# Performance work log

Hardware: AMD Instinct MI355X
Metric: run time of the kernel (lower is better)

Reference implementation:

```python
import jax, jax.numpy as jnp
import numpy as np

SOLVER_STEPS = 10
POINT_DIM = 2
CONTEXT_DIM = 128
HIDDEN_DIM = 256


def setup_inputs() -> dict:
    key = jax.random.key(0)
    ks = jax.random.split(key, 8)
    B, N = 64, 4096
    in_dim = POINT_DIM + 1 + CONTEXT_DIM  # 131
    std = 0.1  # torch nn.init.normal_(std=0.1)
    x = jax.random.normal(ks[0], (B, N, POINT_DIM), jnp.float32)
    context = jax.random.normal(ks[1], (B, CONTEXT_DIM), jnp.float32)
    w1 = std * jax.random.normal(ks[2], (in_dim, HIDDEN_DIM), jnp.float32)
    w2 = std * jax.random.normal(ks[3], (HIDDEN_DIM, HIDDEN_DIM), jnp.float32)
    w3 = std * jax.random.normal(ks[4], (HIDDEN_DIM, HIDDEN_DIM), jnp.float32)
    w4 = std * 0.1 * jax.random.normal(ks[5], (HIDDEN_DIM, POINT_DIM), jnp.float32)  # last layer weight * 0.1
    b1 = jnp.zeros((HIDDEN_DIM,), jnp.float32)
    b2 = jnp.zeros((HIDDEN_DIM,), jnp.float32)
    b3 = jnp.zeros((HIDDEN_DIM,), jnp.float32)
    b4 = jnp.zeros((POINT_DIM,), jnp.float32)
    return {"x": x, "context": context, "w1": w1, "b1": b1, "w2": w2, "b2": b2,
            "w3": w3, "b3": b3, "w4": w4, "b4": b4}


def _mlp(pts, t, ctx, w1, b1, w2, b2, w3, b3, w4, b4):
    # pts: [B,N,2], ctx: [B,N,C] -> velocity [B,N,2]
    B, N, _ = pts.shape
    t_vec = jnp.full((B, N, 1), t, dtype=pts.dtype)
    h = jnp.concatenate([pts, t_vec, ctx], axis=-1)
    h = jax.nn.silu(h @ w1 + b1)  # Swish == silu
    h = jax.nn.silu(h @ w2 + b2)
    h = jax.nn.silu(h @ w3 + b3)
    return h @ w4 + b4


def reference(x, context, w1, b1, w2, b2, w3, b3, w4, b4):
    B, N, D = x.shape
    ctx = jnp.broadcast_to(context[:, None, :], (B, N, context.shape[-1]))
    dt = jnp.asarray(1.0 / SOLVER_STEPS, x.dtype)
    ts = jnp.linspace(0.0, 1.0, SOLVER_STEPS + 1, dtype=x.dtype)[:SOLVER_STEPS]
    e0 = jnp.broadcast_to(jnp.array([1.0, 0.0], x.dtype), x.shape)
    e1 = jnp.broadcast_to(jnp.array([0.0, 1.0], x.dtype), x.shape)

    def step(carry, t_i):
        pts, log_det = carry
        f = lambda p: _mlp(p, t_i, ctx, w1, b1, w2, b2, w3, b3, w4, b4)
        # exact divergence = trace of per-point 2x2 Jacobian via two JVPs
        v, j0 = jax.jvp(f, (pts,), (e0,))
        _, j1 = jax.jvp(f, (pts,), (e1,))
        div = (j0[..., 0] + j1[..., 1])[..., None]  # [B,N,1]
        return (pts + v * dt, log_det + div * dt), None

    init = (x, jnp.zeros((B, N, 1), x.dtype))
    (final_pts, log_det), _ = jax.lax.scan(step, init, ts)
    final_log_det = log_det[..., 0].sum(axis=1, keepdims=True)  # [B,1]
    return final_pts, final_log_det
```

## Files before the change

kernel.cpp:

```cpp
#include <hip/hip_runtime.h>

typedef short bf16x8 __attribute__((ext_vector_type(8)));
typedef float f32x4 __attribute__((ext_vector_type(4)));
typedef float f32x16 __attribute__((ext_vector_type(16)));

#define AS 264
#define T0OFF (32 * AS)
#define T1OFF (64 * AS)

__device__ __forceinline__ unsigned short f2bf(float f) {
    union { float f; unsigned int u; } v; v.f = f;
    unsigned int u = v.u + 0x7FFFu + ((v.u >> 16) & 1u);
    return (unsigned short)(u >> 16);
}
__device__ __forceinline__ unsigned cvtpk(float a, float b) {
    unsigned r;
    asm("v_cvt_pk_bf16_f32 %0, %1, %2" : "=v"(r) : "v"(a), "v"(b));
    return r;
}
__device__ __forceinline__ float bf2f(unsigned int h) {
    union { unsigned int u; float f; } v; v.u = h << 16; return v.f;
}
__device__ __forceinline__ float sigm(float x) {
    return __builtin_amdgcn_rcpf(1.0f + __expf(-x));
}

struct f4s { float v[4]; };
__device__ __forceinline__ f4s ld4(const float* p) {
    float4 t = *(const float4*)p;
    f4s r; r.v[0] = t.x; r.v[1] = t.y; r.v[2] = t.z; r.v[3] = t.w; return r;
}


__global__ void k_base(const float* __restrict__ ctx,
                       const float* __restrict__ w1,
                       const float* __restrict__ b1,
                       float* __restrict__ base) {
    const int b = blockIdx.x, n = threadIdx.x;
    float acc = b1[n];
    for (int c = 0; c < 128; ++c)
        acc += ctx[b * 128 + c] * w1[(3 + c) * 256 + n];
    base[b * 256 + n] = acc;
}

__global__ void k_frag(const float* __restrict__ w,
                       unsigned short* __restrict__ wf) {
    const int t = blockIdx.x * blockDim.x + threadIdx.x;
    const int j = t & 7, lane = (t >> 3) & 63, hb = (t >> 9) & 7, kk = t >> 12;
    const int c = kk * 16 + (lane >> 5) * 8 + j;
    const int h = hb * 32 + (lane & 31);
    wf[t] = f2bf(w[c * 256 + h]);
}

__device__ __forceinline__ void do_gemm32(const unsigned short* __restrict__ wf,
                                          const unsigned short* Asl,
                                          int abase, int wub,
                                          f32x16& aP, f32x16& aT0, f32x16& aT1) {
    const bf16x8* __restrict__ wp = (const bf16x8*)wf;
    bf16x8 buf[4];
#pragma unroll
    for (int i = 0; i < 4; ++i) buf[i] = wp[wub + i * 512];
#pragma unroll 1
    for (int kk = 0; kk < 12; kk += 4) {
#pragma unroll
        for (int u = 0; u < 4; ++u) {
            const int koff = (kk + u) * 16;
            const bf16x8 fP  = *(const bf16x8*)(Asl + abase + koff);
            const bf16x8 fT0 = *(const bf16x8*)(Asl + abase + koff + T0OFF);
            const bf16x8 fT1 = *(const bf16x8*)(Asl + abase + koff + T1OFF);
            aP  = __builtin_amdgcn_mfma_f32_32x32x16_bf16(buf[u], fP,  aP,  0, 0, 0);
            aT0 = __builtin_amdgcn_mfma_f32_32x32x16_bf16(buf[u], fT0, aT0, 0, 0, 0);
            aT1 = __builtin_amdgcn_mfma_f32_32x32x16_bf16(buf[u], fT1, aT1, 0, 0, 0);
            buf[u] = wp[wub + (kk + 4 + u) * 512];
        }
    }
#pragma unroll
    for (int u = 0; u < 4; ++u) {
        const int koff = (12 + u) * 16;
        const bf16x8 fP  = *(const bf16x8*)(Asl + abase + koff);
        const bf16x8 fT0 = *(const bf16x8*)(Asl + abase + koff + T0OFF);
        const bf16x8 fT1 = *(const bf16x8*)(Asl + abase + koff + T1OFF);
        aP  = __builtin_amdgcn_mfma_f32_32x32x16_bf16(buf[u], fP,  aP,  0, 0, 0);
        aT0 = __builtin_amdgcn_mfma_f32_32x32x16_bf16(buf[u], fT0, aT0, 0, 0, 0);
        aT1 = __builtin_amdgcn_mfma_f32_32x32x16_bf16(buf[u], fT1, aT1, 0, 0, 0);
    }
}

__device__ __forceinline__ void el_write32(unsigned short* Asl,
                                           const f32x16& aP, const f32x16& aT0, const f32x16& aT1,
                                           int ebase) {
#pragma unroll
    for (int g = 0; g < 4; ++g) {
        float h[4], t0[4], t1[4];
#pragma unroll
        for (int e = 0; e < 4; ++e) {
            const float pre = aP[4 * g + e];
            const float s = sigm(pre);
            const float hv = pre * s;
            const float dd = fmaf(hv, 1.0f - s, s);
            h[e]  = hv;
            t0[e] = dd * aT0[4 * g + e];
            t1[e] = dd * aT1[4 * g + e];
        }
        uint2 v0, v1, v2;
        v0.x = cvtpk(h[0],  h[1]);  v0.y = cvtpk(h[2],  h[3]);
        v1.x = cvtpk(t0[0], t0[1]); v1.y = cvtpk(t0[2], t0[3]);
        v2.x = cvtpk(t1[0], t1[1]); v2.y = cvtpk(t1[2], t1[3]);
        *(uint2*)(Asl + ebase + 8 * g)         = v0;
        *(uint2*)(Asl + ebase + 8 * g + T0OFF) = v1;
        *(uint2*)(Asl + ebase + 8 * g + T1OFF) = v2;
    }
}

__launch_bounds__(512, 4)
__global__ void k_main(const float* __restrict__ x,
                       const float* __restrict__ w1,
                       const float* __restrict__ b2g,
                       const float* __restrict__ b3g,
                       const float* __restrict__ w4g,
                       const float* __restrict__ b4g,
                       const unsigned short* __restrict__ w2f,
                       const unsigned short* __restrict__ w3f,
                       const float* __restrict__ basep,
                       float* __restrict__ ldacc,
                       float* __restrict__ out) {
    __shared__ unsigned short Asl[96 * AS];
    __shared__ float w1r[3][256];
    __shared__ float basel[256];
    __shared__ float w40[256], w41[256];
    __shared__ float b2l[256], b3l[256];
    __shared__ float px[32][2];
    __shared__ float pld[32];

    const int tid = threadIdx.x;
    const int wg = blockIdx.x;
    const int b = wg >> 7;
    const int n0 = (wg & 127) << 5;

    for (int i = tid; i < 768; i += 512) w1r[i >> 8][i & 255] = w1[i];
    if (tid < 256) {
        basel[tid] = basep[b * 256 + tid];
        w40[tid] = w4g[2 * tid]; w41[tid] = w4g[2 * tid + 1];
        b2l[tid] = b2g[tid];     b3l[tid] = b3g[tid];
    }
    if (tid < 64) ((float*)px)[tid] = x[((b << 12) + n0) * 2 + tid];
    if (tid < 32) pld[tid] = 0.0f;

    const int lane = tid & 63, wave = tid >> 6;
    const int p = lane & 31, kh = lane >> 5;
    const int hb = wave;
    const int abase = p * AS + kh * 8;
    const int ebase = p * AS + hb * 32 + kh * 4;
    const int wub   = hb * 64 + lane;
    const int bbase = hb * 32 + kh * 4;

    const int p4 = tid >> 4;
    const int ic = tid & 15;

    const float b40 = b4g[0], b41 = b4g[1];
    __syncthreads();

#pragma unroll 1
    for (int st = 0; st < 10; ++st) {
        const float ti = 0.1f * (float)st;
        const float x0 = px[p4][0];
        const float x1 = px[p4][1];
#pragma unroll
        for (int g = 0; g < 4; ++g) {
            const int cb = g * 64 + (ic << 2);
            const f4s wa = ld4(&w1r[0][cb]);
            const f4s wb = ld4(&w1r[1][cb]);
            const f4s wc = ld4(&w1r[2][cb]);
            const f4s bs = ld4(&basel[cb]);
            float hf[4], t0f[4], t1f[4];
#pragma unroll
            for (int e = 0; e < 4; ++e) {
                const float pre = x0 * wa.v[e] + x1 * wb.v[e] + ti * wc.v[e] + bs.v[e];
                const float s = sigm(pre);
                const float h = pre * s;
                const float d = fmaf(h, 1.0f - s, s);
                hf[e]  = h;
                t0f[e] = d * wa.v[e];
                t1f[e] = d * wb.v[e];
            }
            uint2 v0, v1, v2;
            v0.x = cvtpk(hf[0],  hf[1]);  v0.y = cvtpk(hf[2],  hf[3]);
            v1.x = cvtpk(t0f[0], t0f[1]); v1.y = cvtpk(t0f[2], t0f[3]);
            v2.x = cvtpk(t1f[0], t1f[1]); v2.y = cvtpk(t1f[2], t1f[3]);
            *(uint2*)(Asl + p4 * AS + cb) = v0;
            *(uint2*)(Asl + T0OFF + p4 * AS + cb) = v1;
            *(uint2*)(Asl + T1OFF + p4 * AS + cb) = v2;
        }
        __syncthreads();

        f32x16 aP, aT0, aT1;
#pragma unroll
        for (int g = 0; g < 4; ++g) {
            const float4 bv = *(const float4*)&b2l[bbase + 8 * g];
            aP[4 * g + 0] = bv.x; aP[4 * g + 1] = bv.y;
            aP[4 * g + 2] = bv.z; aP[4 * g + 3] = bv.w;
        }
#pragma unroll
        for (int r = 0; r < 16; ++r) { aT0[r] = 0.f; aT1[r] = 0.f; }
        do_gemm32(w2f, Asl, abase, wub, aP, aT0, aT1);
        __syncthreads();
        el_write32(Asl, aP, aT0, aT1, ebase);
        __syncthreads();

#pragma unroll
        for (int g = 0; g < 4; ++g) {
            const float4 bv = *(const float4*)&b3l[bbase + 8 * g];
            aP[4 * g + 0] = bv.x; aP[4 * g + 1] = bv.y;
            aP[4 * g + 2] = bv.z; aP[4 * g + 3] = bv.w;
        }
#pragma unroll
        for (int r = 0; r < 16; ++r) { aT0[r] = 0.f; aT1[r] = 0.f; }
        do_gemm32(w3f, Asl, abase, wub, aP, aT0, aT1);
        __syncthreads();
        el_write32(Asl, aP, aT0, aT1, ebase);
        __syncthreads();

        {
            float v0 = 0.f, v1 = 0.f, j00 = 0.f, j11 = 0.f;
#pragma unroll
            for (int g = 0; g < 4; ++g) {
                const int cb = g * 64 + (ic << 2);
                const uint2 hv  = *(const uint2*)(Asl + p4 * AS + cb);
                const uint2 t0v = *(const uint2*)(Asl + T0OFF + p4 * AS + cb);
                const uint2 t1v = *(const uint2*)(Asl + T1OFF + p4 * AS + cb);
                const f4s wa = ld4(&w40[cb]);
                const f4s wb = ld4(&w41[cb]);
                const unsigned hu[4]  = { hv.x & 0xffffu,  hv.x >> 16,  hv.y & 0xffffu,  hv.y >> 16 };
                const unsigned t0u[4] = { t0v.x & 0xffffu, t0v.x >> 16, t0v.y & 0xffffu, t0v.y >> 16 };
                const unsigned t1u[4] = { t1v.x & 0xffffu, t1v.x >> 16, t1v.y & 0xffffu, t1v.y >> 16 };
#pragma unroll
                for (int e = 0; e < 4; ++e) {
                    const float h = bf2f(hu[e]);
                    v0  += h * wa.v[e];
                    v1  += h * wb.v[e];
                    j00 += bf2f(t0u[e]) * wa.v[e];
                    j11 += bf2f(t1u[e]) * wb.v[e];
                }
            }
#pragma unroll
            for (int o = 1; o < 16; o <<= 1) {
                v0  += __shfl_xor(v0, o);
                v1  += __shfl_xor(v1, o);
                j00 += __shfl_xor(j00, o);
                j11 += __shfl_xor(j11, o);
            }
            if (ic == 0) {
                px[p4][0] += 0.1f * (v0 + b40);
                px[p4][1] += 0.1f * (v1 + b41);
                pld[p4]   += 0.1f * (j00 + j11);
            }
        }
    }

    if (ic == 0) {
        out[((b << 12) + n0 + p4) * 2]     = px[p4][0];
        out[((b << 12) + n0 + p4) * 2 + 1] = px[p4][1];
    }
    __syncthreads();
    if (wave == 0) {
        float v = (lane < 32) ? pld[lane] : 0.0f;
#pragma unroll
        for (int o = 32; o > 0; o >>= 1) v += __shfl_xor(v, o);
        if (lane == 0) atomicAdd(ldacc + b, v);
    }
}

__global__ void k_fin(const float* __restrict__ ldacc, float* __restrict__ out) {
    out[524288 + threadIdx.x] = ldacc[threadIdx.x];
}

extern "C" void kernel_launch(void* const* d_in, const int* in_sizes, int n_in,
                              void* d_out, int out_size, void* d_ws, size_t ws_size,
                              hipStream_t stream) {
    const float* x   = (const float*)d_in[0];
    const float* ctx = (const float*)d_in[1];
    const float* w1  = (const float*)d_in[2];
    const float* b1  = (const float*)d_in[3];
    const float* w2  = (const float*)d_in[4];
    const float* b2  = (const float*)d_in[5];
    const float* w3  = (const float*)d_in[6];
    const float* b3  = (const float*)d_in[7];
    const float* w4  = (const float*)d_in[8];
    const float* b4  = (const float*)d_in[9];

    char* ws = (char*)d_ws;
    unsigned short* w2f = (unsigned short*)ws;
    unsigned short* w3f = (unsigned short*)(ws + 131072);
    float* basep = (float*)(ws + 262144);
    float* ldacc = (float*)(ws + 327680);
    float* out = (float*)d_out;

    hipMemsetAsync(ldacc, 0, 64 * sizeof(float), stream);
    k_base<<<dim3(64), dim3(256), 0, stream>>>(ctx, w1, b1, basep);
    k_frag<<<dim3(128), dim3(512), 0, stream>>>(w2, w2f);
    k_frag<<<dim3(128), dim3(512), 0, stream>>>(w3, w3f);
    k_main<<<dim3(8192), dim3(512), 0, stream>>>(x, w1, b2, b3, w4, b4, w2f, w3f, basep, ldacc, out);
    k_fin<<<dim3(1), dim3(64), 0, stream>>>(ldacc, out);
}
```

Before: 2.401 ms.

## Halve block to four waves, each computing two hidden column blocks

The main kernel now launches 256 threads per block, and each wave computes two 32-wide hidden column blocks instead of one. Each A fragment read from LDS is therefore reused across six MFMAs, which halves LDS A-fragment traffic per MFMA. The first-layer and output-reduction loops are reshaped for 8 threads per point. The cost is double the accumulator registers (six 16-float accumulators), and launch bounds drop to 256 threads with 2 blocks, which may reduce occupancy and latency hiding.

```diff
diff --git a/kernel.cpp b/kernel.cpp
--- a/kernel.cpp
+++ b/kernel.cpp
@@ -52,39 +52,18 @@
     wf[t] = f2bf(w[c * 256 + h]);
 }
 
-__device__ __forceinline__ void do_gemm32(const unsigned short* __restrict__ wf,
-                                          const unsigned short* Asl,
-                                          int abase, int wub,
-                                          f32x16& aP, f32x16& aT0, f32x16& aT1) {
-    const bf16x8* __restrict__ wp = (const bf16x8*)wf;
-    bf16x8 buf[4];
-#pragma unroll
-    for (int i = 0; i < 4; ++i) buf[i] = wp[wub + i * 512];
-#pragma unroll 1
-    for (int kk = 0; kk < 12; kk += 4) {
-#pragma unroll
-        for (int u = 0; u < 4; ++u) {
-            const int koff = (kk + u) * 16;
-            const bf16x8 fP  = *(const bf16x8*)(Asl + abase + koff);
-            const bf16x8 fT0 = *(const bf16x8*)(Asl + abase + koff + T0OFF);
-            const bf16x8 fT1 = *(const bf16x8*)(Asl + abase + koff + T1OFF);
-            aP  = __builtin_amdgcn_mfma_f32_32x32x16_bf16(buf[u], fP,  aP,  0, 0, 0);
-            aT0 = __builtin_amdgcn_mfma_f32_32x32x16_bf16(buf[u], fT0, aT0, 0, 0, 0);
-            aT1 = __builtin_amdgcn_mfma_f32_32x32x16_bf16(buf[u], fT1, aT1, 0, 0, 0);
-            buf[u] = wp[wub + (kk + 4 + u) * 512];
-        }
-    }
-#pragma unroll
-    for (int u = 0; u < 4; ++u) {
-        const int koff = (12 + u) * 16;
-        const bf16x8 fP  = *(const bf16x8*)(Asl + abase + koff);
-        const bf16x8 fT0 = *(const bf16x8*)(Asl + abase + koff + T0OFF);
-        const bf16x8 fT1 = *(const bf16x8*)(Asl + abase + koff + T1OFF);
-        aP  = __builtin_amdgcn_mfma_f32_32x32x16_bf16(buf[u], fP,  aP,  0, 0, 0);
-        aT0 = __builtin_amdgcn_mfma_f32_32x32x16_bf16(buf[u], fT0, aT0, 0, 0, 0);
-        aT1 = __builtin_amdgcn_mfma_f32_32x32x16_bf16(buf[u], fT1, aT1, 0, 0, 0);
-    }
-}
+#define MFMA6(koff, w0, w1)                                                        \
+    {                                                                              \
+        const bf16x8 fP  = *(const bf16x8*)(Asl + abase + (koff));                 \
+        const bf16x8 fT0 = *(const bf16x8*)(Asl + abase + (koff) + T0OFF);         \
+        const bf16x8 fT1 = *(const bf16x8*)(Asl + abase + (koff) + T1OFF);         \
+        aP0  = __builtin_amdgcn_mfma_f32_32x32x16_bf16(w0, fP,  aP0,  0, 0, 0);    \
+        aT00 = __builtin_amdgcn_mfma_f32_32x32x16_bf16(w0, fT0, aT00, 0, 0, 0);    \
+        aT10 = __builtin_amdgcn_mfma_f32_32x32x16_bf16(w0, fT1, aT10, 0, 0, 0);    \
+        aP1  = __builtin_amdgcn_mfma_f32_32x32x16_bf16(w1, fP,  aP1,  0, 0, 0);    \
+        aT01 = __builtin_amdgcn_mfma_f32_32x32x16_bf16(w1, fT0, aT01, 0, 0, 0);    \
+        aT11 = __builtin_amdgcn_mfma_f32_32x32x16_bf16(w1, fT1, aT11, 0, 0, 0);    \
+    }
 
 __device__ __forceinline__ void el_write32(unsigned short* Asl,
                                            const f32x16& aP, const f32x16& aT0, const f32x16& aT1,
@@ -112,7 +91,7 @@
     }
 }
 
-__launch_bounds__(512, 4)
+__launch_bounds__(256, 2)
 __global__ void k_main(const float* __restrict__ x,
                        const float* __restrict__ w1,
                        const float* __restrict__ b2g,
@@ -137,8 +116,8 @@
     const int b = wg >> 7;
     const int n0 = (wg & 127) << 5;
 
-    for (int i = tid; i < 768; i += 512) w1r[i >> 8][i & 255] = w1[i];
-    if (tid < 256) {
+    for (int i = tid; i < 768; i += 256) w1r[i >> 8][i & 255] = w1[i];
+    {
         basel[tid] = basep[b * 256 + tid];
         w40[tid] = w4g[2 * tid]; w41[tid] = w4g[2 * tid + 1];
         b2l[tid] = b2g[tid];     b3l[tid] = b3g[tid];
@@ -148,14 +127,17 @@
 
     const int lane = tid & 63, wave = tid >> 6;
     const int p = lane & 31, kh = lane >> 5;
-    const int hb = wave;
-    const int abase = p * AS + kh * 8;
-    const int ebase = p * AS + hb * 32 + kh * 4;
-    const int wub   = hb * 64 + lane;
-    const int bbase = hb * 32 + kh * 4;
-
-    const int p4 = tid >> 4;
-    const int ic = tid & 15;
+    const int hb0 = 2 * wave, hb1 = 2 * wave + 1;
+    const int abase  = p * AS + kh * 8;
+    const int ebase0 = p * AS + hb0 * 32 + kh * 4;
+    const int ebase1 = p * AS + hb1 * 32 + kh * 4;
+    const int wub0   = hb0 * 64 + lane;
+    const int wub1   = hb1 * 64 + lane;
+    const int bbase0 = hb0 * 32 + kh * 4;
+    const int bbase1 = hb1 * 32 + kh * 4;
+
+    const int p4 = tid >> 3;
+    const int ic = tid & 7;
 
     const float b40 = b4g[0], b41 = b4g[1];
     __syncthreads();
@@ -166,8 +148,8 @@
         const float x0 = px[p4][0];
         const float x1 = px[p4][1];
 #pragma unroll
-        for (int g = 0; g < 4; ++g) {
-            const int cb = g * 64 + (ic << 2);
+        for (int g = 0; g < 8; ++g) {
+            const int cb = g * 32 + (ic << 2);
             const f4s wa = ld4(&w1r[0][cb]);
             const f4s wb = ld4(&w1r[1][cb]);
             const f4s wc = ld4(&w1r[2][cb]);
@@ -193,38 +175,78 @@
         }
         __syncthreads();
 
-        f32x16 aP, aT0, aT1;
+        f32x16 aP0, aT00, aT10, aP1, aT01, aT11;
 #pragma unroll
         for (int g = 0; g < 4; ++g) {
-            const float4 bv = *(const float4*)&b2l[bbase + 8 * g];
-            aP[4 * g + 0] = bv.x; aP[4 * g + 1] = bv.y;
-            aP[4 * g + 2] = bv.z; aP[4 * g + 3] = bv.w;
-        }
-#pragma unroll
-        for (int r = 0; r < 16; ++r) { aT0[r] = 0.f; aT1[r] = 0.f; }
-        do_gemm32(w2f, Asl, abase, wub, aP, aT0, aT1);
-        __syncthreads();
-        el_write32(Asl, aP, aT0, aT1, ebase);
+            const float4 bv0 = *(const float4*)&b2l[bbase0 + 8 * g];
+            const float4 bv1 = *(const float4*)&b2l[bbase1 + 8 * g];
+            aP0[4 * g + 0] = bv0.x; aP0[4 * g + 1] = bv0.y;
+            aP0[4 * g + 2] = bv0.z; aP0[4 * g + 3] = bv0.w;
+            aP1[4 * g + 0] = bv1.x; aP1[4 * g + 1] = bv1.y;
+            aP1[4 * g + 2] = bv1.z; aP1[4 * g + 3] = bv1.w;
+        }
+#pragma unroll
+        for (int r = 0; r < 16; ++r) { aT00[r] = 0.f; aT10[r] = 0.f; aT01[r] = 0.f; aT11[r] = 0.f; }
+        {
+            const bf16x8* __restrict__ wp = (const bf16x8*)w2f;
+            bf16x8 b0[4], b1[4];
+#pragma unroll
+            for (int i = 0; i < 4; ++i) { b0[i] = wp[wub0 + i * 512]; b1[i] = wp[wub1 + i * 512]; }
+#pragma unroll 1
+            for (int kk = 0; kk < 12; kk += 4) {
+#pragma unroll
+                for (int u = 0; u < 4; ++u) {
+                    MFMA6((kk + u) * 16, b0[u], b1[u]);
+                    b0[u] = wp[wub0 + (kk + 4 + u) * 512];
+                    b1[u] = wp[wub1 + (kk + 4 + u) * 512];
+                }
+            }
+#pragma unroll
+            for (int u = 0; u < 4; ++u) MFMA6((12 + u) * 16, b0[u], b1[u]);
+        }
+        __syncthreads();
+        el_write32(Asl, aP0, aT00, aT10, ebase0);
+        el_write32(Asl, aP1, aT01, aT11, ebase1);
         __syncthreads();
 
 #pragma unroll
         for (int g = 0; g < 4; ++g) {
-            const float4 bv = *(const float4*)&b3l[bbase + 8 * g];
-            aP[4 * g + 0] = bv.x; aP[4 * g + 1] = bv.y;
-            aP[4 * g + 2] = bv.z; aP[4 * g + 3] = bv.w;
-        }
-#pragma unroll
-        for (int r = 0; r < 16; ++r) { aT0[r] = 0.f; aT1[r] = 0.f; }
-        do_gemm32(w3f, Asl, abase, wub, aP, aT0, aT1);
-        __syncthreads();
-        el_write32(Asl, aP, aT0, aT1, ebase);
+            const float4 bv0 = *(const float4*)&b3l[bbase0 + 8 * g];
+            const float4 bv1 = *(const float4*)&b3l[bbase1 + 8 * g];
+            aP0[4 * g + 0] = bv0.x; aP0[4 * g + 1] = bv0.y;
+            aP0[4 * g + 2] = bv0.z; aP0[4 * g + 3] = bv0.w;
+            aP1[4 * g + 0] = bv1.x; aP1[4 * g + 1] = bv1.y;
+            aP1[4 * g + 2] = bv1.z; aP1[4 * g + 3] = bv1.w;
+        }
+#pragma unroll
+        for (int r = 0; r < 16; ++r) { aT00[r] = 0.f; aT10[r] = 0.f; aT01[r] = 0.f; aT11[r] = 0.f; }
+        {
+            const bf16x8* __restrict__ wp = (const bf16x8*)w3f;
+            bf16x8 b0[4], b1[4];
+#pragma unroll
+            for (int i = 0; i < 4; ++i) { b0[i] = wp[wub0 + i * 512]; b1[i] = wp[wub1 + i * 512]; }
+#pragma unroll 1
+            for (int kk = 0; kk < 12; kk += 4) {
+#pragma unroll
+                for (int u = 0; u < 4; ++u) {
+                    MFMA6((kk + u) * 16, b0[u], b1[u]);
+                    b0[u] = wp[wub0 + (kk + 4 + u) * 512];
+                    b1[u] = wp[wub1 + (kk + 4 + u) * 512];
+                }
+            }
+#pragma unroll
+            for (int u = 0; u < 4; ++u) MFMA6((12 + u) * 16, b0[u], b1[u]);
+        }
+        __syncthreads();
+        el_write32(Asl, aP0, aT00, aT10, ebase0);
+        el_write32(Asl, aP1, aT01, aT11, ebase1);
         __syncthreads();
 
         {
             float v0 = 0.f, v1 = 0.f, j00 = 0.f, j11 = 0.f;
 #pragma unroll
-            for (int g = 0; g < 4; ++g) {
-                const int cb = g * 64 + (ic << 2);
+            for (int g = 0; g < 8; ++g) {
+                const int cb = g * 32 + (ic << 2);
                 const uint2 hv  = *(const uint2*)(Asl + p4 * AS + cb);
                 const uint2 t0v = *(const uint2*)(Asl + T0OFF + p4 * AS + cb);
                 const uint2 t1v = *(const uint2*)(Asl + T1OFF + p4 * AS + cb);
@@ -243,7 +265,7 @@
                 }
             }
 #pragma unroll
-            for (int o = 1; o < 16; o <<= 1) {
+            for (int o = 1; o < 8; o <<= 1) {
                 v0  += __shfl_xor(v0, o);
                 v1  += __shfl_xor(v1, o);
                 j00 += __shfl_xor(j00, o);
@@ -299,6 +321,6 @@
     k_base<<<dim3(64), dim3(256), 0, stream>>>(ctx, w1, b1, basep);
     k_frag<<<dim3(128), dim3(512), 0, stream>>>(w2, w2f);
     k_frag<<<dim3(128), dim3(512), 0, stream>>>(w3, w3f);
-    k_main<<<dim3(8192), dim3(512), 0, stream>>>(x, w1, b2, b3, w4, b4, w2f, w3f, basep, ldacc, out);
+    k_main<<<dim3(8192), dim3(256), 0, stream>>>(x, w1, b2, b3, w4, b4, w2f, w3f, basep, ldacc, out);
     k_fin<<<dim3(1), dim3(64), 0, stream>>>(ldacc, out);
 }
```

Measured after the change: 2.236 ms. 6.8% less time.
